# Kernel optimization log

Measured on AMD Instinct MI355X. Metric: run time of the kernel, lower is better.

Reference implementation:

```python
import jax, jax.numpy as jnp
import numpy as np

V, E, H, T, B = 50000, 300, 1024, 512, 32   # vocab, embed, hidden, seq, batch
A_DIM, R, MLP_H, C = 350, 30, 512, 2        # attention_dim, num_aspects, mlp_hidden, classes


def setup_inputs() -> dict:
    key = jax.random.key(0)
    ks = jax.random.split(key, 10)
    inp = jax.random.randint(ks[0], (B, T), 0, V)
    lens = jax.random.randint(ks[1], (B,), 1, T + 1)  # variable lengths, >=1
    W_emb = jax.random.normal(ks[2], (V, E), dtype=jnp.float32) * 0.1
    W_ih = jax.random.normal(ks[3], (2, 4 * H, E), dtype=jnp.float32) * 0.02  # [dir, 4h, E]
    W_hh = jax.random.normal(ks[4], (2, 4 * H, H), dtype=jnp.float32) * 0.02
    b_ih = jnp.zeros((2, 4 * H), dtype=jnp.float32)
    b_hh = jnp.zeros((2, 4 * H), dtype=jnp.float32)
    W1 = jax.random.normal(ks[5], (A_DIM, 2 * H), dtype=jnp.float32) * 0.02
    W2 = jax.random.normal(ks[6], (R, A_DIM), dtype=jnp.float32) * 0.02
    W_mlp = jax.random.normal(ks[7], (MLP_H, R * 2 * H), dtype=jnp.float32) * 0.01
    b_mlp = jnp.zeros((MLP_H,), dtype=jnp.float32)
    W_dec = jax.random.uniform(ks[8], (C, MLP_H), dtype=jnp.float32, minval=-0.1, maxval=0.1)
    b_dec = jnp.zeros((C,), dtype=jnp.float32)
    return dict(inp=inp, lens=lens, W_emb=W_emb, W_ih=W_ih, W_hh=W_hh, b_ih=b_ih,
                b_hh=b_hh, W1=W1, W2=W2, W_mlp=W_mlp, b_mlp=b_mlp, W_dec=W_dec, b_dec=b_dec)


def _lstm_dir(xw, W_hh, reverse):
    """xw: [T,B,4h] (input projection precomputed); PyTorch gate order i,f,g,o."""
    h0 = jnp.zeros((xw.shape[1], W_hh.shape[1]), xw.dtype)
    c0 = h0

    def step(carry, xt):
        h, c = carry
        g = xt + h @ W_hh.T
        i, f, gg, o = jnp.split(g, 4, axis=-1)
        c = jax.nn.sigmoid(f) * c + jax.nn.sigmoid(i) * jnp.tanh(gg)
        h = jax.nn.sigmoid(o) * jnp.tanh(c)
        return (h, c), h

    _, hs = jax.lax.scan(step, (h0, c0), xw, reverse=reverse)
    return hs  # [T,B,h]


def reference(inp, lens, W_emb, W_ih, W_hh, b_ih, b_hh, W1, W2, W_mlp, b_mlp, W_dec, b_dec):
    x = W_emb[inp]                         # [B,T,E] embedding lookup
    xt = x.transpose(1, 0, 2)              # [T,B,E]
    bias = b_ih + b_hh                     # [2,4h]
    h_f = _lstm_dir(xt @ W_ih[0].T + bias[0], W_hh[0], False)
    h_b = _lstm_dir(xt @ W_ih[1].T + bias[1], W_hh[1], True)
    out = jnp.concatenate([h_f, h_b], axis=-1).transpose(1, 0, 2)  # [B,T,2h]

    # Masked per-sample self-attention (vectorized over the ragged loop)
    mask = jnp.arange(T)[None, :] < lens[:, None]                  # [B,T]
    s = jnp.tanh(out @ W1.T) @ W2.T                                # [B,T,R]
    s = jnp.where(mask[..., None], s, -1e9)
    A = jax.nn.softmax(s, axis=1).transpose(0, 2, 1)               # [B,R,T], rows sum to 1 over valid t
    M = jnp.einsum('brt,bth->brh', A, out)                         # [B,R,2h]
    feats = M.reshape(M.shape[0], -1)                              # [B, R*2h]

    # Frobenius orthogonality penalty: mean_i ||A_i A_i^T - I||_F^2
    AAT = jnp.einsum('brt,bst->brs', A, A)
    I = jnp.eye(R, dtype=AAT.dtype)
    penal = jnp.mean(jnp.sum((AAT - I) ** 2, axis=(1, 2)))

    hid = jax.nn.relu(feats @ W_mlp.T + b_mlp)
    decoded = jax.nn.softmax(hid @ W_dec.T + b_dec, axis=-1)       # [B,C]
    return decoded, penal
```

## Files before the change

kernel.cpp:

```cpp
#include <hip/hip_runtime.h>
#include <stdint.h>

typedef __attribute__((ext_vector_type(8))) short short8;
typedef __attribute__((ext_vector_type(4))) float f32x4;
typedef __attribute__((ext_vector_type(4))) unsigned int u32x4;

#define B_    32
#define T_    512
#define E_    300
#define KE_   384
#define H_    1024
#define G4_   4096
#define R_    30
#define AD_   350
#define AC_   384
#define MH_   512
#define FEAT_ 61440
#define NU_   16
#define DTICK 16ull

__device__ __forceinline__ unsigned short f2bu(float f) {
  unsigned int x = __builtin_bit_cast(unsigned int, f);
  x += 0x7fffu + ((x >> 16) & 1u);
  return (unsigned short)(x >> 16);
}
__device__ __forceinline__ float b2f(unsigned short u) {
  return __builtin_bit_cast(float, (unsigned int)u << 16);
}
__device__ __forceinline__ float sigm(float x) {
  return __builtin_amdgcn_rcpf(1.f + __expf(-x));
}
__device__ __forceinline__ float tanh_fast(float x) {
  return 1.f - 2.f * __builtin_amdgcn_rcpf(1.f + __expf(2.f * x));
}

#define BULK8G_ISS(b0p, b1p, FL)                                                \
  asm volatile(                                                                 \
      "global_load_dwordx4 %0, %8, off " FL "\n\t"                              \
      "global_load_dwordx4 %1, %8, off offset:1024 " FL "\n\t"                  \
      "global_load_dwordx4 %2, %8, off offset:2048 " FL "\n\t"                  \
      "global_load_dwordx4 %3, %8, off offset:3072 " FL "\n\t"                  \
      "global_load_dwordx4 %4, %9, off " FL "\n\t"                              \
      "global_load_dwordx4 %5, %9, off offset:1024 " FL "\n\t"                  \
      "global_load_dwordx4 %6, %9, off offset:2048 " FL "\n\t"                  \
      "global_load_dwordx4 %7, %9, off offset:3072 " FL                         \
      : "=&v"(q0), "=&v"(q1), "=&v"(q2), "=&v"(q3),                             \
        "=&v"(q4), "=&v"(q5), "=&v"(q6), "=&v"(q7)                              \
      : "v"(b0p), "v"(b1p)                                                      \
      : "memory")

#define BULK8G(b0p, b1p, FL)                                                    \
  do {                                                                          \
    BULK8G_ISS(b0p, b1p, FL);                                                   \
    asm volatile("s_waitcnt vmcnt(0)" ::: "memory");                            \
    __builtin_amdgcn_sched_barrier(0);                                          \
  } while (0)

#define VAL8(BAD)                                                               \
  {                                                                             \
    u32x4 o01 = q0 | q1, o23 = q2 | q3, o45 = q4 | q5, o67 = q6 | q7;           \
    u32x4 ov4 = (o01 | o23) | (o45 | o67);                                      \
    unsigned ovv = (ov4[0] | ov4[1]) | (ov4[2] | ov4[3]);                       \
    BAD = (ovv & 0x40004000u) != 0;                                             \
  }

__global__ void k0_prep(const int* __restrict__ inp, const float* __restrict__ W_emb,
                        const float* __restrict__ W_ih, const float* __restrict__ W1,
                        const float* __restrict__ W_mlp,
                        unsigned short* __restrict__ xb, unsigned short* __restrict__ wihb,
                        unsigned short* __restrict__ w1b, unsigned short* __restrict__ wmlpb) {
  const int N1 = 16384 * KE_;
  const int N2 = 8192 * KE_;
  const int N3 = AC_ * 2048;
  const int N4 = MH_ * FEAT_;
  const int NT = N1 + N2 + N3 + N4;
  for (int i = blockIdx.x * blockDim.x + threadIdx.x; i < NT; i += gridDim.x * blockDim.x) {
    if (i < N1) {
      int row = i / KE_, e = i - row * KE_;
      float v = (e < E_) ? W_emb[(size_t)inp[row] * E_ + e] : 0.f;
      xb[i] = f2bu(v);
    } else if (i < N1 + N2) {
      int j = i - N1;
      int rw = j / KE_, e = j - rw * KE_;
      float v = (e < E_) ? W_ih[(size_t)rw * E_ + e] : 0.f;
      wihb[j] = f2bu(v);
    } else if (i < N1 + N2 + N3) {
      int j = i - N1 - N2;
      int a = j >> 11, k = j & 2047;
      float v = (a < AD_) ? W1[(size_t)a * 2048 + k] : 0.f;
      w1b[j] = f2bu(v);
    } else {
      int j = i - N1 - N2 - N3;
      wmlpb[j] = f2bu(W_mlp[j]);
    }
  }
}

__global__ __launch_bounds__(256, 1) void k2_rnn(const float* __restrict__ Whh,
                                                 const unsigned short* __restrict__ wihb,
                                                 const unsigned short* __restrict__ xb,
                                                 const float* __restrict__ b_ih,
                                                 const float* __restrict__ b_hh,
                                                 unsigned short* __restrict__ outb,
                                                 unsigned short* __restrict__ hpub) {
  const int dir = blockIdx.x >> 7;
  const int w = (blockIdx.x >> 1) & 63;
  const int bh = blockIdx.x & 1;
  const int tid = threadIdx.x;
  const int wid = tid >> 6, lane = tid & 63;
  const int l15 = lane & 15, lg = lane >> 4;

  __shared__ float Gp[4][4][16][17];
  __shared__ __align__(16) unsigned short htmp[16][16];

  short8 afr[4][8];
  {
    const int kq = wid << 8;
#pragma unroll
    for (int g = 0; g < 4; ++g) {
      const float* wp = Whh + ((size_t)dir * G4_ + g * H_ + w * NU_ + l15) * H_ + kq + lg * 8;
#pragma unroll
      for (int ktl = 0; ktl < 8; ++ktl) {
        float4 f0 = *(const float4*)(wp + ktl * 32);
        float4 f1 = *(const float4*)(wp + ktl * 32 + 4);
        short8 s;
        s[0] = (short)f2bu(f0.x); s[1] = (short)f2bu(f0.y);
        s[2] = (short)f2bu(f0.z); s[3] = (short)f2bu(f0.w);
        s[4] = (short)f2bu(f1.x); s[5] = (short)f2bu(f1.y);
        s[6] = (short)f2bu(f1.z); s[7] = (short)f2bu(f1.w);
        afr[g][ktl] = s;
      }
    }
  }

  const int kqx = wid * 96;
  short8 axr[4][3];
#pragma unroll
  for (int g = 0; g < 4; ++g) {
    const unsigned short* xp = wihb + ((size_t)dir * G4_ + g * H_ + w * NU_ + l15) * KE_ + kqx + lg * 8;
#pragma unroll
    for (int kt = 0; kt < 3; ++kt) axr[g][kt] = *(const short8*)(xp + kt * 32);
  }

  const int u = tid >> 4;
  const int b = tid & 15;

  float bsum[4];
#pragma unroll
  for (int g = 0; g < 4; ++g) {
    int row = dir * G4_ + g * H_ + w * NU_ + u;
    bsum[g] = b_ih[row] + b_hh[row];
  }

  const size_t hlane = (size_t)(wid * 16 + (lg >> 1)) * 256 + l15 * 16 + (lg & 1) * 8;
  const size_t hpoll = (size_t)(wid * 16 + (lane & 15)) * 256;

  float cst = 0.f;
  unsigned long long pprev = __builtin_amdgcn_s_memrealtime();

#pragma unroll 1
  for (int s = 0; s < T_; ++s) {
    const int t = dir ? (T_ - 1 - s) : s;

    f32x4 acc[4];
#pragma unroll
    for (int g = 0; g < 4; ++g) acc[g] = (f32x4){0.f, 0.f, 0.f, 0.f};

    {
      short8 xbf[3];
#pragma unroll
      for (int kt = 0; kt < 3; ++kt)
        xbf[kt] = *(const short8*)(xb + ((size_t)(bh * 16 + l15) * T_ + t) * KE_ + kqx + kt * 32 + lg * 8);
#pragma unroll
      for (int kt = 0; kt < 3; ++kt)
#pragma unroll
        for (int g = 0; g < 4; ++g)
          acc[g] = __builtin_amdgcn_mfma_f32_16x16x32_bf16(axr[g][kt], xbf[kt], acc[g], 0, 0, 0);
    }
    __builtin_amdgcn_sched_barrier(0);

    if (s > 0) {
      const int tsrc = dir ? t + 1 : t - 1;
      const unsigned short* hbase = hpub + ((size_t)(dir * T_ + tsrc) * 2 + bh) * 16384;
      const unsigned short* B0 = hbase + hlane;
      const unsigned short* B1 = B0 + 4096;
      u32x4 q0, q1, q2, q3, q4, q5, q6, q7;

      {
        unsigned long long tgt = pprev + DTICK;
        unsigned long long now;
        do { now = __builtin_amdgcn_s_memrealtime(); } while (now < tgt);
      }

      BULK8G(B0, B1, "sc0");
      bool bad; VAL8(bad);
      if (__builtin_expect(bad, 0)) {
        const unsigned short* sp = hbase + hpoll;
        unsigned v;
        int guard = 0;
        for (;;) {
          asm volatile("global_load_dword %0, %1, off sc0 sc1\n\ts_waitcnt vmcnt(0)"
                       : "=v"(v) : "v"(sp) : "memory");
          if (__all(!(v & 0x40004000u))) break;
          if (++guard > 50000) break;
        }
        int g2 = 0;
        do {
          BULK8G(B0, B1, "sc0 sc1");
          VAL8(bad);
        } while (bad && ++g2 < 50000);
      }

      short8 bf[8];
      bf[0] = __builtin_bit_cast(short8, q0); bf[1] = __builtin_bit_cast(short8, q1);
      bf[2] = __builtin_bit_cast(short8, q2); bf[3] = __builtin_bit_cast(short8, q3);
      bf[4] = __builtin_bit_cast(short8, q4); bf[5] = __builtin_bit_cast(short8, q5);
      bf[6] = __builtin_bit_cast(short8, q6); bf[7] = __builtin_bit_cast(short8, q7);

#pragma unroll
      for (int ktl = 0; ktl < 8; ++ktl)
#pragma unroll
        for (int g = 0; g < 4; ++g)
          acc[g] = __builtin_amdgcn_mfma_f32_16x16x32_bf16(afr[g][ktl], bf[ktl], acc[g], 0, 0, 0);
    }

#pragma unroll
    for (int g = 0; g < 4; ++g)
#pragma unroll
      for (int j = 0; j < 4; ++j)
        Gp[wid][g][l15][lg * 4 + j] = acc[g][j];
    __syncthreads();

    {
      float gi = Gp[0][0][b][u] + Gp[1][0][b][u] + Gp[2][0][b][u] + Gp[3][0][b][u] + bsum[0];
      float gf = Gp[0][1][b][u] + Gp[1][1][b][u] + Gp[2][1][b][u] + Gp[3][1][b][u] + bsum[1];
      float gg = Gp[0][2][b][u] + Gp[1][2][b][u] + Gp[2][2][b][u] + Gp[3][2][b][u] + bsum[2];
      float go = Gp[0][3][b][u] + Gp[1][3][b][u] + Gp[2][3][b][u] + Gp[3][3][b][u] + bsum[3];
      cst = sigm(gf) * cst + sigm(gi) * tanh_fast(gg);
      float hv = sigm(go) * tanh_fast(cst);
      htmp[b][u] = f2bu(hv);
    }
    __syncthreads();

    pprev = __builtin_amdgcn_s_memrealtime();
    if (tid < 64) {
      int bb = tid >> 2, q = tid & 3;
      uint2 v = *(const uint2*)&htmp[bb][q * 4];
      unsigned short* hp = hpub + ((size_t)(dir * T_ + t) * 2 + bh) * 16384 + (size_t)w * 256 + bb * 16 + q * 4;
      asm volatile("global_store_dwordx2 %0, %1, off sc0 sc1" :: "v"(hp), "v"(v) : "memory");
      *(uint2*)(outb + ((size_t)(bh * 16 + bb) * T_ + t) * 2048 + dir * H_ + w * NU_ + q * 4) = v;
    }
  }
}

__global__ __launch_bounds__(256, 1) void k3_s1(const unsigned short* __restrict__ outb,
                                                const unsigned short* __restrict__ w1b,
                                                unsigned short* __restrict__ th1) {
  const int rb = blockIdx.x;
  const int wid = threadIdx.x >> 6, lane = threadIdx.x & 63;
  const int m = wid & 1, nh = wid >> 1;
  const int l15 = lane & 15, lg = lane >> 4;

  f32x4 acc[12];
#pragma unroll
  for (int nt = 0; nt < 12; ++nt) acc[nt] = (f32x4){0.f, 0.f, 0.f, 0.f};

  const unsigned short* arow = outb + ((size_t)rb * 32 + m * 16 + l15) * 2048;
  for (int kt = 0; kt < 64; ++kt) {
    short8 af = *(const short8*)(arow + kt * 32 + lg * 8);
#pragma unroll
    for (int nt = 0; nt < 12; ++nt) {
      int col = nh * 192 + nt * 16 + l15;
      short8 bf = *(const short8*)(w1b + (size_t)col * 2048 + kt * 32 + lg * 8);
      acc[nt] = __builtin_amdgcn_mfma_f32_16x16x32_bf16(af, bf, acc[nt], 0, 0, 0);
    }
  }
#pragma unroll
  for (int nt = 0; nt < 12; ++nt) {
#pragma unroll
    for (int j = 0; j < 4; ++j) {
      int row = rb * 32 + m * 16 + lg * 4 + j;
      int col = nh * 192 + nt * 16 + l15;
      th1[(size_t)row * AC_ + col] = f2bu(tanh_fast(acc[nt][j]));
    }
  }
}

__global__ void k4_s2(const unsigned short* __restrict__ th1, const float* __restrict__ W2,
                      float* __restrict__ abuf) {
  int idx = blockIdx.x * 256 + threadIdx.x;
  int row = idx >> 5, r = idx & 31;
  if (r >= R_) return;
  const unsigned short* tp = th1 + (size_t)row * AC_;
  const float* wp = W2 + r * AD_;
  float acc = 0.f;
  for (int a = 0; a < AD_; ++a) acc = fmaf(b2f(tp[a]), wp[a], acc);
  int b = row >> 9, t = row & 511;
  abuf[((size_t)b * R_ + r) * T_ + t] = acc;
}

__global__ void k5_sm(float* __restrict__ abuf, const int* __restrict__ lens) {
  int wv = blockIdx.x * 4 + (threadIdx.x >> 6);
  int lane = threadIdx.x & 63;
  if (wv >= B_ * R_) return;
  int b = wv / R_, r = wv % R_;
  int len = lens[b];
  float* row = abuf + ((size_t)b * R_ + r) * T_;
  float v[8];
  float mx = -1e30f;
#pragma unroll
  for (int i = 0; i < 8; ++i) {
    int t = lane + i * 64;
    float x = (t < len) ? row[t] : -1e30f;
    v[i] = x;
    mx = fmaxf(mx, x);
  }
#pragma unroll
  for (int o = 32; o > 0; o >>= 1) mx = fmaxf(mx, __shfl_xor(mx, o));
  float sum = 0.f;
#pragma unroll
  for (int i = 0; i < 8; ++i) {
    float e = (v[i] > -1e29f) ? __expf(v[i] - mx) : 0.f;
    v[i] = e;
    sum += e;
  }
#pragma unroll
  for (int o = 32; o > 0; o >>= 1) sum += __shfl_xor(sum, o);
  float inv = 1.f / sum;
#pragma unroll
  for (int i = 0; i < 8; ++i) row[lane + i * 64] = v[i] * inv;
}

__global__ __launch_bounds__(256) void k6_m(const float* __restrict__ abuf,
                                            const unsigned short* __restrict__ outb,
                                            unsigned short* __restrict__ mbuf) {
  int b = blockIdx.x >> 4, hb = blockIdx.x & 15;
  __shared__ float As[R_ * T_];
  for (int i = threadIdx.x; i < R_ * T_; i += 256) As[i] = abuf[(size_t)b * R_ * T_ + i];
  __syncthreads();
  int h = threadIdx.x & 127, rh = threadIdx.x >> 7;
  float acc[15];
#pragma unroll
  for (int rr = 0; rr < 15; ++rr) acc[rr] = 0.f;
  const unsigned short* op = outb + (size_t)b * T_ * 2048 + hb * 128 + h;
  for (int t = 0; t < T_; ++t) {
    float vv = b2f(op[(size_t)t * 2048]);
#pragma unroll
    for (int rr = 0; rr < 15; ++rr) acc[rr] = fmaf(As[(rh * 15 + rr) * T_ + t], vv, acc[rr]);
  }
#pragma unroll
  for (int rr = 0; rr < 15; ++rr)
    mbuf[(size_t)b * FEAT_ + (size_t)(rh * 15 + rr) * 2048 + hb * 128 + h] = f2bu(acc[rr]);
}

__global__ __launch_bounds__(256) void k7_pen(const float* __restrict__ abuf,
                                              float* __restrict__ penp) {
  int b = blockIdx.x;
  __shared__ float As[R_ * 515];
  __shared__ float red[256];
  for (int i = threadIdx.x; i < R_ * T_; i += 256) {
    int r = i >> 9, t = i & 511;
    As[r * 515 + t] = abuf[(size_t)b * R_ * T_ + i];
  }
  __syncthreads();
  float psum = 0.f;
  for (int p = threadIdx.x; p < R_ * R_; p += 256) {
    int r = p / R_, s = p % R_;
    const float* pr = As + r * 515;
    const float* ps = As + s * 515;
    float d = 0.f;
    for (int t = 0; t < T_; ++t) d = fmaf(pr[t], ps[t], d);
    d -= (r == s) ? 1.f : 0.f;
    psum += d * d;
  }
  red[threadIdx.x] = psum;
  __syncthreads();
  for (int o = 128; o > 0; o >>= 1) {
    if (threadIdx.x < o) red[threadIdx.x] += red[threadIdx.x + o];
    __syncthreads();
  }
  if (threadIdx.x == 0) penp[b] = red[0];
}

__global__ __launch_bounds__(256, 1) void k8_mlp(const unsigned short* __restrict__ wmlpb,
                                                 const unsigned short* __restrict__ mbuf,
                                                 float* __restrict__ hid) {
  const int mblk = blockIdx.x >> 4, kblk = blockIdx.x & 15;
  const int wid = threadIdx.x >> 6, lane = threadIdx.x & 63;
  const int l15 = lane & 15, lg = lane >> 4;
  const int kq = kblk * 3840 + wid * 960;

  f32x4 acc[2][2];
#pragma unroll
  for (int i = 0; i < 2; ++i)
#pragma unroll
    for (int j = 0; j < 2; ++j) acc[i][j] = (f32x4){0.f, 0.f, 0.f, 0.f};

  const unsigned short* ap0 = wmlpb + (size_t)(mblk * 32 + l15) * FEAT_ + kq + lg * 8;
  const unsigned short* ap1 = ap0 + (size_t)16 * FEAT_;
  const unsigned short* bp0 = mbuf + (size_t)l15 * FEAT_ + kq + lg * 8;
  const unsigned short* bp1 = bp0 + (size_t)16 * FEAT_;
  for (int kt = 0; kt < 30; ++kt) {
    short8 a0 = *(const short8*)(ap0 + kt * 32);
    short8 a1 = *(const short8*)(ap1 + kt * 32);
    short8 b0 = *(const short8*)(bp0 + kt * 32);
    short8 b1 = *(const short8*)(bp1 + kt * 32);
    acc[0][0] = __builtin_amdgcn_mfma_f32_16x16x32_bf16(a0, b0, acc[0][0], 0, 0, 0);
    acc[0][1] = __builtin_amdgcn_mfma_f32_16x16x32_bf16(a0, b1, acc[0][1], 0, 0, 0);
    acc[1][0] = __builtin_amdgcn_mfma_f32_16x16x32_bf16(a1, b0, acc[1][0], 0, 0, 0);
    acc[1][1] = __builtin_amdgcn_mfma_f32_16x16x32_bf16(a1, b1, acc[1][1], 0, 0, 0);
  }

  __shared__ float red[4][32][33];
#pragma unroll
  for (int mi = 0; mi < 2; ++mi)
#pragma unroll
    for (int ni = 0; ni < 2; ++ni)
#pragma unroll
      for (int j = 0; j < 4; ++j)
        red[wid][mi * 16 + lg * 4 + j][ni * 16 + l15] = acc[mi][ni][j];
  __syncthreads();

  int m = threadIdx.x >> 3, b4 = (threadIdx.x & 7) * 4;
#pragma unroll
  for (int k = 0; k < 4; ++k) {
    int bb = b4 + k;
    float s = red[0][m][bb] + red[1][m][bb] + red[2][m][bb] + red[3][m][bb];
    atomicAdd(&hid[(size_t)bb * MH_ + mblk * 32 + m], s);
  }
}

__global__ void k9_out(const float* __restrict__ hid, const float* __restrict__ b_mlp,
                       const float* __restrict__ W_dec, const float* __restrict__ b_dec,
                       const float* __restrict__ penp, float* __restrict__ out) {
  int tid = threadIdx.x;
  if (tid < 64) {
    int b = tid >> 1, c = tid & 1;
    const float* hp = hid + (size_t)b * MH_;
    const float* wp = W_dec + (size_t)c * MH_;
    float acc = b_dec[c];
    for (int k = 0; k < MH_; ++k) {
      float hk = fmaxf(hp[k] + b_mlp[k], 0.f);
      acc = fmaf(hk, wp[k], acc);
    }
    float other = __shfl_xor(acc, 1);
    float mx = fmaxf(acc, other);
    float e = __expf(acc - mx), eo = __expf(other - mx);
    out[b * 2 + c] = e / (e + eo);
  } else if (tid == 64) {
    float s = 0.f;
    for (int b = 0; b < B_; ++b) s += penp[b];
    out[64] = s * (1.f / 32.f);
  }
}

extern "C" void kernel_launch(void* const* d_in, const int* in_sizes, int n_in,
                              void* d_out, int out_size, void* d_ws, size_t ws_size,
                              hipStream_t stream) {
  const int* inp = (const int*)d_in[0];
  const int* lens = (const int*)d_in[1];
  const float* W_emb = (const float*)d_in[2];
  const float* W_ih = (const float*)d_in[3];
  const float* W_hh = (const float*)d_in[4];
  const float* b_ih = (const float*)d_in[5];
  const float* b_hh = (const float*)d_in[6];
  const float* W1 = (const float*)d_in[7];
  const float* W2 = (const float*)d_in[8];
  const float* W_mlp = (const float*)d_in[9];
  const float* b_mlp = (const float*)d_in[10];
  const float* W_dec = (const float*)d_in[11];
  const float* b_dec = (const float*)d_in[12];
  float* out = (float*)d_out;

  char* ws = (char*)d_ws;
  size_t off = 0;
  auto take = [&](size_t bytes) -> char* {
    char* p = ws + off;
    off = (off + bytes + 255) & ~(size_t)255;
    return p;
  };
  unsigned short* outb = (unsigned short*)take((size_t)B_ * T_ * 2048 * 2);
  unsigned short* hpub = (unsigned short*)take((size_t)2 * T_ * 2 * 16384 * 2);
  unsigned short* xb = (unsigned short*)take((size_t)16384 * KE_ * 2);
  unsigned short* wihb = (unsigned short*)take((size_t)8192 * KE_ * 2);
  unsigned short* w1b = (unsigned short*)take((size_t)AC_ * 2048 * 2);
  unsigned short* wmlpb = (unsigned short*)take((size_t)MH_ * FEAT_ * 2);
  unsigned short* th1 = (unsigned short*)take((size_t)16384 * AC_ * 2);
  float* abuf = (float*)take((size_t)B_ * R_ * T_ * 4);
  unsigned short* mbuf = (unsigned short*)take((size_t)B_ * FEAT_ * 2);
  float* penp = (float*)take(B_ * 4);
  float* hid = (float*)take((size_t)B_ * MH_ * 4);

  if (off > ws_size) {
    hipMemsetAsync(d_out, 0xFF, (size_t)out_size * 4, stream);
    return;
  }

  hipMemsetAsync(hpub, 0xFF, (size_t)2 * T_ * 2 * 16384 * 2, stream);
  hipMemsetAsync(hid, 0, (size_t)B_ * MH_ * 4, stream);

  k0_prep<<<2048, 256, 0, stream>>>(inp, W_emb, W_ih, W1, W_mlp, xb, wihb, w1b, wmlpb);
  k2_rnn<<<256, 256, 0, stream>>>(W_hh, wihb, xb, b_ih, b_hh, outb, hpub);
  k3_s1<<<512, 256, 0, stream>>>(outb, w1b, th1);
  k4_s2<<<2048, 256, 0, stream>>>(th1, W2, abuf);
  k5_sm<<<240, 256, 0, stream>>>(abuf, lens);
  k6_m<<<512, 256, 0, stream>>>(abuf, outb, mbuf);
  k7_pen<<<32, 256, 0, stream>>>(abuf, penp);
  k8_mlp<<<256, 256, 0, stream>>>(wmlpb, mbuf, hid);
  k9_out<<<1, 128, 0, stream>>>(hid, b_mlp, W_dec, b_dec, penp, out);
}
```

Baseline: 2.065 ms.

## Fuse attention-score stages, softmax with penalty, and W_mlp bf16 conversion

```diff
diff --git a/kernel.cpp b/kernel.cpp
--- a/kernel.cpp
+++ b/kernel.cpp
@@ -66,14 +66,12 @@
 
 __global__ void k0_prep(const int* __restrict__ inp, const float* __restrict__ W_emb,
                         const float* __restrict__ W_ih, const float* __restrict__ W1,
-                        const float* __restrict__ W_mlp,
                         unsigned short* __restrict__ xb, unsigned short* __restrict__ wihb,
-                        unsigned short* __restrict__ w1b, unsigned short* __restrict__ wmlpb) {
+                        unsigned short* __restrict__ w1b) {
   const int N1 = 16384 * KE_;
   const int N2 = 8192 * KE_;
   const int N3 = AC_ * 2048;
-  const int N4 = MH_ * FEAT_;
-  const int NT = N1 + N2 + N3 + N4;
+  const int NT = N1 + N2 + N3;
   for (int i = blockIdx.x * blockDim.x + threadIdx.x; i < NT; i += gridDim.x * blockDim.x) {
     if (i < N1) {
       int row = i / KE_, e = i - row * KE_;
@@ -84,14 +82,11 @@
       int rw = j / KE_, e = j - rw * KE_;
       float v = (e < E_) ? W_ih[(size_t)rw * E_ + e] : 0.f;
       wihb[j] = f2bu(v);
-    } else if (i < N1 + N2 + N3) {
+    } else {
       int j = i - N1 - N2;
       int a = j >> 11, k = j & 2047;
       float v = (a < AD_) ? W1[(size_t)a * 2048 + k] : 0.f;
       w1b[j] = f2bu(v);
-    } else {
-      int j = i - N1 - N2 - N3;
-      wmlpb[j] = f2bu(W_mlp[j]);
     }
   }
 }
@@ -255,12 +250,15 @@
 
 __global__ __launch_bounds__(256, 1) void k3_s1(const unsigned short* __restrict__ outb,
                                                 const unsigned short* __restrict__ w1b,
-                                                unsigned short* __restrict__ th1) {
+                                                const float* __restrict__ W2,
+                                                float* __restrict__ abuf) {
   const int rb = blockIdx.x;
   const int wid = threadIdx.x >> 6, lane = threadIdx.x & 63;
   const int m = wid & 1, nh = wid >> 1;
   const int l15 = lane & 15, lg = lane >> 4;
 
+  __shared__ unsigned short th_l[32][392];
+
   f32x4 acc[12];
 #pragma unroll
   for (int nt = 0; nt < 12; ++nt) acc[nt] = (f32x4){0.f, 0.f, 0.f, 0.f};
@@ -279,56 +277,95 @@
   for (int nt = 0; nt < 12; ++nt) {
 #pragma unroll
     for (int j = 0; j < 4; ++j) {
-      int row = rb * 32 + m * 16 + lg * 4 + j;
+      int lr = m * 16 + lg * 4 + j;
       int col = nh * 192 + nt * 16 + l15;
-      th1[(size_t)row * AC_ + col] = f2bu(tanh_fast(acc[nt][j]));
-    }
-  }
-}
-
-__global__ void k4_s2(const unsigned short* __restrict__ th1, const float* __restrict__ W2,
-                      float* __restrict__ abuf) {
-  int idx = blockIdx.x * 256 + threadIdx.x;
-  int row = idx >> 5, r = idx & 31;
-  if (r >= R_) return;
-  const unsigned short* tp = th1 + (size_t)row * AC_;
-  const float* wp = W2 + r * AD_;
-  float acc = 0.f;
-  for (int a = 0; a < AD_; ++a) acc = fmaf(b2f(tp[a]), wp[a], acc);
-  int b = row >> 9, t = row & 511;
-  abuf[((size_t)b * R_ + r) * T_ + t] = acc;
-}
-
-__global__ void k5_sm(float* __restrict__ abuf, const int* __restrict__ lens) {
-  int wv = blockIdx.x * 4 + (threadIdx.x >> 6);
-  int lane = threadIdx.x & 63;
-  if (wv >= B_ * R_) return;
-  int b = wv / R_, r = wv % R_;
-  int len = lens[b];
-  float* row = abuf + ((size_t)b * R_ + r) * T_;
-  float v[8];
-  float mx = -1e30f;
-#pragma unroll
-  for (int i = 0; i < 8; ++i) {
-    int t = lane + i * 64;
-    float x = (t < len) ? row[t] : -1e30f;
-    v[i] = x;
-    mx = fmaxf(mx, x);
-  }
-#pragma unroll
-  for (int o = 32; o > 0; o >>= 1) mx = fmaxf(mx, __shfl_xor(mx, o));
-  float sum = 0.f;
-#pragma unroll
-  for (int i = 0; i < 8; ++i) {
-    float e = (v[i] > -1e29f) ? __expf(v[i] - mx) : 0.f;
-    v[i] = e;
-    sum += e;
-  }
-#pragma unroll
-  for (int o = 32; o > 0; o >>= 1) sum += __shfl_xor(sum, o);
-  float inv = 1.f / sum;
-#pragma unroll
-  for (int i = 0; i < 8; ++i) row[lane + i * 64] = v[i] * inv;
+      th_l[lr][col] = f2bu(tanh_fast(acc[nt][j]));
+    }
+  }
+  __syncthreads();
+
+  for (int task = threadIdx.x; task < 32 * R_; task += 256) {
+    int lr = task / R_, r = task - lr * R_;
+    const float* wp = W2 + r * AD_;
+    const unsigned short* tp = &th_l[lr][0];
+    float s = 0.f;
+#pragma unroll 2
+    for (int a = 0; a < AD_; ++a) s = fmaf(b2f(tp[a]), wp[a], s);
+    int grow = rb * 32 + lr;
+    int b = grow >> 9, t = grow & 511;
+    abuf[((size_t)b * R_ + r) * T_ + t] = s;
+  }
+}
+
+__global__ __launch_bounds__(512, 1) void k5_sm(float* __restrict__ abuf,
+                                                const int* __restrict__ lens,
+                                                float* __restrict__ penp) {
+  const int b = blockIdx.x;
+  const int tid = threadIdx.x;
+  __shared__ float As[R_ * 515];
+  __shared__ float red[512];
+
+  for (int i = tid; i < R_ * T_; i += 512) {
+    int r = i >> 9, t = i & 511;
+    As[r * 515 + t] = abuf[(size_t)b * R_ * T_ + i];
+  }
+  __syncthreads();
+
+  const int len = lens[b];
+  const int wv = tid >> 6, lane = tid & 63;
+#pragma unroll 1
+  for (int k = 0; k < 4; ++k) {
+    int r = wv * 4 + k;
+    if (r >= R_) break;
+    float* row = As + r * 515;
+    float v[8];
+    float mx = -1e30f;
+#pragma unroll
+    for (int i = 0; i < 8; ++i) {
+      int t = lane + i * 64;
+      float x = (t < len) ? row[t] : -1e30f;
+      v[i] = x;
+      mx = fmaxf(mx, x);
+    }
+#pragma unroll
+    for (int o = 32; o > 0; o >>= 1) mx = fmaxf(mx, __shfl_xor(mx, o));
+    float sum = 0.f;
+#pragma unroll
+    for (int i = 0; i < 8; ++i) {
+      float e = (v[i] > -1e29f) ? __expf(v[i] - mx) : 0.f;
+      v[i] = e;
+      sum += e;
+    }
+#pragma unroll
+    for (int o = 32; o > 0; o >>= 1) sum += __shfl_xor(sum, o);
+    float inv = 1.f / sum;
+#pragma unroll
+    for (int i = 0; i < 8; ++i) {
+      int t = lane + i * 64;
+      float e = v[i] * inv;
+      row[t] = e;
+      abuf[(size_t)b * R_ * T_ + r * T_ + t] = e;
+    }
+  }
+  __syncthreads();
+
+  float psum = 0.f;
+  for (int task = tid; task < R_ * R_; task += 512) {
+    int r = task / R_, s2 = task - (task / R_) * R_;
+    const float* pr = As + r * 515;
+    const float* ps = As + s2 * 515;
+    float d = 0.f;
+    for (int t = 0; t < T_; ++t) d = fmaf(pr[t], ps[t], d);
+    d -= (r == s2) ? 1.f : 0.f;
+    psum += d * d;
+  }
+  red[tid] = psum;
+  __syncthreads();
+  for (int o = 256; o > 0; o >>= 1) {
+    if (tid < o) red[tid] += red[tid + o];
+    __syncthreads();
+  }
+  if (tid == 0) penp[b] = red[0];
 }
 
 __global__ __launch_bounds__(256) void k6_m(const float* __restrict__ abuf,
@@ -353,36 +390,7 @@
     mbuf[(size_t)b * FEAT_ + (size_t)(rh * 15 + rr) * 2048 + hb * 128 + h] = f2bu(acc[rr]);
 }
 
-__global__ __launch_bounds__(256) void k7_pen(const float* __restrict__ abuf,
-                                              float* __restrict__ penp) {
-  int b = blockIdx.x;
-  __shared__ float As[R_ * 515];
-  __shared__ float red[256];
-  for (int i = threadIdx.x; i < R_ * T_; i += 256) {
-    int r = i >> 9, t = i & 511;
-    As[r * 515 + t] = abuf[(size_t)b * R_ * T_ + i];
-  }
-  __syncthreads();
-  float psum = 0.f;
-  for (int p = threadIdx.x; p < R_ * R_; p += 256) {
-    int r = p / R_, s = p % R_;
-    const float* pr = As + r * 515;
-    const float* ps = As + s * 515;
-    float d = 0.f;
-    for (int t = 0; t < T_; ++t) d = fmaf(pr[t], ps[t], d);
-    d -= (r == s) ? 1.f : 0.f;
-    psum += d * d;
-  }
-  red[threadIdx.x] = psum;
-  __syncthreads();
-  for (int o = 128; o > 0; o >>= 1) {
-    if (threadIdx.x < o) red[threadIdx.x] += red[threadIdx.x + o];
-    __syncthreads();
-  }
-  if (threadIdx.x == 0) penp[b] = red[0];
-}
-
-__global__ __launch_bounds__(256, 1) void k8_mlp(const unsigned short* __restrict__ wmlpb,
+__global__ __launch_bounds__(256, 1) void k8_mlp(const float* __restrict__ W_mlp,
                                                  const unsigned short* __restrict__ mbuf,
                                                  float* __restrict__ hid) {
   const int mblk = blockIdx.x >> 4, kblk = blockIdx.x & 15;
@@ -396,13 +404,24 @@
 #pragma unroll
     for (int j = 0; j < 2; ++j) acc[i][j] = (f32x4){0.f, 0.f, 0.f, 0.f};
 
-  const unsigned short* ap0 = wmlpb + (size_t)(mblk * 32 + l15) * FEAT_ + kq + lg * 8;
-  const unsigned short* ap1 = ap0 + (size_t)16 * FEAT_;
+  const float* ap0f = W_mlp + (size_t)(mblk * 32 + l15) * FEAT_ + kq + lg * 8;
+  const float* ap1f = ap0f + (size_t)16 * FEAT_;
   const unsigned short* bp0 = mbuf + (size_t)l15 * FEAT_ + kq + lg * 8;
   const unsigned short* bp1 = bp0 + (size_t)16 * FEAT_;
   for (int kt = 0; kt < 30; ++kt) {
-    short8 a0 = *(const short8*)(ap0 + kt * 32);
-    short8 a1 = *(const short8*)(ap1 + kt * 32);
+    float4 f0 = *(const float4*)(ap0f + kt * 32);
+    float4 f1 = *(const float4*)(ap0f + kt * 32 + 4);
+    float4 g0 = *(const float4*)(ap1f + kt * 32);
+    float4 g1 = *(const float4*)(ap1f + kt * 32 + 4);
+    short8 a0, a1;
+    a0[0] = (short)f2bu(f0.x); a0[1] = (short)f2bu(f0.y);
+    a0[2] = (short)f2bu(f0.z); a0[3] = (short)f2bu(f0.w);
+    a0[4] = (short)f2bu(f1.x); a0[5] = (short)f2bu(f1.y);
+    a0[6] = (short)f2bu(f1.z); a0[7] = (short)f2bu(f1.w);
+    a1[0] = (short)f2bu(g0.x); a1[1] = (short)f2bu(g0.y);
+    a1[2] = (short)f2bu(g0.z); a1[3] = (short)f2bu(g0.w);
+    a1[4] = (short)f2bu(g1.x); a1[5] = (short)f2bu(g1.y);
+    a1[6] = (short)f2bu(g1.z); a1[7] = (short)f2bu(g1.w);
     short8 b0 = *(const short8*)(bp0 + kt * 32);
     short8 b1 = *(const short8*)(bp1 + kt * 32);
     acc[0][0] = __builtin_amdgcn_mfma_f32_16x16x32_bf16(a0, b0, acc[0][0], 0, 0, 0);
@@ -484,8 +503,6 @@
   unsigned short* xb = (unsigned short*)take((size_t)16384 * KE_ * 2);
   unsigned short* wihb = (unsigned short*)take((size_t)8192 * KE_ * 2);
   unsigned short* w1b = (unsigned short*)take((size_t)AC_ * 2048 * 2);
-  unsigned short* wmlpb = (unsigned short*)take((size_t)MH_ * FEAT_ * 2);
-  unsigned short* th1 = (unsigned short*)take((size_t)16384 * AC_ * 2);
   float* abuf = (float*)take((size_t)B_ * R_ * T_ * 4);
   unsigned short* mbuf = (unsigned short*)take((size_t)B_ * FEAT_ * 2);
   float* penp = (float*)take(B_ * 4);
@@ -499,13 +516,11 @@
   hipMemsetAsync(hpub, 0xFF, (size_t)2 * T_ * 2 * 16384 * 2, stream);
   hipMemsetAsync(hid, 0, (size_t)B_ * MH_ * 4, stream);
 
-  k0_prep<<<2048, 256, 0, stream>>>(inp, W_emb, W_ih, W1, W_mlp, xb, wihb, w1b, wmlpb);
+  k0_prep<<<2048, 256, 0, stream>>>(inp, W_emb, W_ih, W1, xb, wihb, w1b);
   k2_rnn<<<256, 256, 0, stream>>>(W_hh, wihb, xb, b_ih, b_hh, outb, hpub);
-  k3_s1<<<512, 256, 0, stream>>>(outb, w1b, th1);
-  k4_s2<<<2048, 256, 0, stream>>>(th1, W2, abuf);
-  k5_sm<<<240, 256, 0, stream>>>(abuf, lens);
+  k3_s1<<<512, 256, 0, stream>>>(outb, w1b, W2, abuf);
+  k5_sm<<<32, 512, 0, stream>>>(abuf, lens, penp);
   k6_m<<<512, 256, 0, stream>>>(abuf, outb, mbuf);
-  k7_pen<<<32, 256, 0, stream>>>(abuf, penp);
-  k8_mlp<<<256, 256, 0, stream>>>(wmlpb, mbuf, hid);
+  k8_mlp<<<256, 256, 0, stream>>>(W_mlp, mbuf, hid);
   k9_out<<<1, 128, 0, stream>>>(hid, b_mlp, W_dec, b_dec, penp, out);
 }
```

Measured after the change: 2.031 ms. No clear change (-1.6%).
